# Performance work log

Hardware: AMD Instinct MI355X
Metric: run time of the kernel (lower is better)

The kernel has to match this reference:

```python
import jax, jax.numpy as jnp
import numpy as np

EPS_SINK = 0.01   # SinkhornDistance eps
N_ITERS = 20      # fixed iteration count (original: max 100 with host-side early exit)
BN_EPS = 1e-5


def _conv(x, w, b):
    # NCHW 3x3 (or 1x1) conv, SAME padding
    y = jax.lax.conv_general_dilated(x, w, (1, 1), 'SAME',
                                     dimension_numbers=('NCHW', 'OIHW', 'NCHW'))
    return y + b[None, :, None, None]


def _bn_train(x, gamma, beta):
    # BatchNorm2d in training mode: batch statistics over (N,H,W)
    m = jnp.mean(x, axis=(0, 2, 3), keepdims=True)
    v = jnp.var(x, axis=(0, 2, 3), keepdims=True)
    return gamma[None, :, None, None] * (x - m) * jax.lax.rsqrt(v + BN_EPS) + beta[None, :, None, None]


def _calc_mean_std(f, eps=1e-5):
    m = jnp.mean(f, axis=(2, 3), keepdims=True)
    s = jnp.sqrt(jnp.var(f, axis=(2, 3), keepdims=True) + eps)
    return m, s


def _sinkhorn_pi(x, y, eps):
    # x: [b, n, d] content points, y: [b, m, d] style points. Cosine-distance cost.
    xn = x / jnp.linalg.norm(x, axis=-1, keepdims=True)
    yn = y / jnp.linalg.norm(y, axis=-1, keepdims=True)
    C = 1.0 - jnp.einsum('bnd,bmd->bnm', xn, yn)          # [b, n, m]
    b, n, m = C.shape
    log_mu = jnp.log(jnp.full((b, n), 1.0 / n) + 1e-8)
    log_nu = jnp.log(jnp.full((b, m), 1.0 / m) + 1e-8)

    def Mmat(u, v):
        # (-C + u_i + v_j) / eps
        return (-C + u[..., None] + v[..., None, :]) / eps

    def step(carry, _):
        u, v = carry
        u = eps * (log_mu - jax.scipy.special.logsumexp(Mmat(u, v), axis=-1)) + u
        v = eps * (log_nu - jax.scipy.special.logsumexp(Mmat(u, v), axis=-2)) + v
        return (u, v), None

    (u, v), _ = jax.lax.scan(step, (jnp.zeros((b, n)), jnp.zeros((b, m))), None, length=N_ITERS)
    return jnp.exp(Mmat(u, v))                             # transport plan pi


def setup_inputs() -> dict:
    key = jax.random.key(0)
    ks = jax.random.split(key, 16)
    bs, dim, h, w = 4, 512, 32, 32
    s = 0.05
    return {
        'content_feat': jax.random.normal(ks[0], (bs, dim, h, w), jnp.float32),
        'style_feat':   jax.random.normal(ks[1], (bs, dim, h, w), jnp.float32),
        # alpha_predictor (version 1): conv(1024->256,3x3) ReLU BN, conv(256->256,3x3) ReLU BN, conv(256->512,3x3)
        'w1': jax.random.normal(ks[2], (256, 1024, 3, 3), jnp.float32) * s,
        'b1': jnp.zeros((256,), jnp.float32),
        'g1': jnp.ones((256,), jnp.float32),
        'be1': jnp.zeros((256,), jnp.float32),
        'w2': jax.random.normal(ks[3], (256, 256, 3, 3), jnp.float32) * s,
        'b2': jnp.zeros((256,), jnp.float32),
        'g2': jnp.ones((256,), jnp.float32),
        'be2': jnp.zeros((256,), jnp.float32),
        'w3': jax.random.normal(ks[4], (512, 256, 3, 3), jnp.float32) * s,
        'b3': jnp.zeros((512,), jnp.float32),
        # stand-in decoder head: 3x3 conv 512->3 (decoder is an external injected module)
        'dec_w': jax.random.normal(ks[5], (3, 512, 3, 3), jnp.float32) * s,
        'dec_b': jnp.zeros((3,), jnp.float32),
    }


def reference(content_feat, style_feat, w1, b1, g1, be1, w2, b2, g2, be2, w3, b3, dec_w, dec_b):
    bs, dim, h, w = content_feat.shape
    cf = content_feat.reshape(bs, dim, h * w).transpose(0, 2, 1)   # [b, hw, d]
    sf = style_feat.reshape(bs, dim, h * w).transpose(0, 2, 1)
    pi = _sinkhorn_pi(cf, sf, EPS_SINK) * (h * w)                  # style_assign: pi * h * w
    t = jnp.einsum('bnm,bmd->bnd', pi, sf).transpose(0, 2, 1).reshape(bs, dim, h, w)
    cm, cs = _calc_mean_std(content_feat)
    c_normed = (content_feat - cm) / cs
    a = _bn_train(jax.nn.relu(_conv(jnp.concatenate([t, content_feat], axis=1), w1, b1)), g1, be1)
    a = _bn_train(jax.nn.relu(_conv(a, w2, b2)), g2, be2)
    alpha = _conv(a, w3, b3)
    t = alpha * c_normed + t
    g_t = _conv(t, dec_w, dec_b)
    return g_t
```

## Files before the change

### kernel.cpp

```cpp
#include <hip/hip_runtime.h>

typedef unsigned short u16;
typedef unsigned int u32;
typedef float f32x4 __attribute__((ext_vector_type(4)));
typedef short bf16x8 __attribute__((ext_vector_type(8)));

#define DEV static __device__ __forceinline__

DEV float bf2f(u16 u){ union{float f; u32 i;} x; x.i = ((u32)u) << 16; return x.f; }
DEV u16 f2bf(float f){ union{float f; u32 i;} x; x.f = f; u32 u = x.i;
  return (u16)((u + 0x7fffu + ((u >> 16) & 1u)) >> 16); }
DEV u16 f2h(float f){ _Float16 h = (_Float16)f; u16 u; __builtin_memcpy(&u, &h, 2); return u; }
DEV float h2f(u16 u){ _Float16 h; __builtin_memcpy(&h, &u, 2); return (float)h; }
DEV uint4 pack8(const u16* s){ uint4 v;
  v.x = (u32)s[0] | ((u32)s[1]<<16); v.y = (u32)s[2] | ((u32)s[3]<<16);
  v.z = (u32)s[4] | ((u32)s[5]<<16); v.w = (u32)s[6] | ((u32)s[7]<<16); return v; }
DEV f32x4 mfma16(bf16x8 a, bf16x8 b, f32x4 c){
  return __builtin_amdgcn_mfma_f32_16x16x32_bf16(a, b, c, 0, 0, 0);
}
DEV bf16x8 ldfrag(const u16* p){ return *(const bf16x8*)p; }

constexpr float SCL = 144.269504088896341f;
constexpr float LOG2MU = -9.99998522680257f;

constexpr size_t MB = 1ull << 20;
constexpr size_t OFF_G    = 0;
constexpr size_t OFF_GT   = 8*MB;
constexpr size_t OFF_U    = 16*MB;
constexpr size_t OFF_V    = OFF_U   + (16<<10);
constexpr size_t OFF_INC  = OFF_V   + (16<<10);
constexpr size_t OFF_INS  = OFF_INC + (16<<10);
constexpr size_t OFF_CNM  = OFF_INS + (16<<10);
constexpr size_t OFF_CNIS = OFF_CNM + (8<<10);
constexpr size_t OFF_BNS  = OFF_CNIS+ (8<<10);
constexpr size_t OFF_PNP  = OFF_BNS + (4<<10);
constexpr size_t OFF_CFH  = 17*MB;
constexpr size_t OFF_CFL  = 21*MB;
constexpr size_t OFF_SFH  = 25*MB;
constexpr size_t OFF_SFL  = 29*MB;
constexpr size_t OFF_SNB  = 33*MB;
constexpr size_t OFF_TN   = 37*MB;
constexpr size_t OFF_TCP  = 45*MB;
constexpr size_t OFF_W1P  = 53*MB;
constexpr size_t OFF_W2P  = OFF_W1P + 9*256*1024*2;
constexpr size_t OFF_W3P  = OFF_W2P + 9*256*256*2;
constexpr size_t OFF_WDP  = OFF_W3P + 9*512*256*2;
constexpr size_t OFF_PIP  = 62*MB;
constexpr size_t OFF_Z1  = 17*MB;
constexpr size_t OFF_A1P = 25*MB;
constexpr size_t OFF_Z2  = 27*MB;
constexpr size_t OFF_A2P = 35*MB;
constexpr size_t OFF_T2P = 17*MB;

__global__ void pack_all_k(const float* __restrict__ w1, const float* __restrict__ w2,
                           const float* __restrict__ w3, const float* __restrict__ wd,
                           u16* __restrict__ w1p, u16* __restrict__ w2p,
                           u16* __restrict__ w3p, u16* __restrict__ wdp){
  int blk = blockIdx.x;
  const float* w; u16* wp; int CI, NCK, rel;
  if (blk < 512){ w = w1; wp = w1p; CI = 1024; NCK = 32; rel = blk; }
  else if (blk < 640){ w = w2; wp = w2p; CI = 256; NCK = 8; rel = blk - 512; }
  else if (blk < 896){ w = w3; wp = w3p; CI = 256; NCK = 8; rel = blk - 640; }
  else {
    int o = (blk - 896)*256 + threadIdx.x;
    int ci = o & 511; int r = o >> 9; int co = r & 15; int tap = r >> 4;
    wdp[o] = f2bf((co < 3) ? wd[(size_t)(co*512 + ci)*9 + tap] : 0.f);
    return;
  }
  int g = rel / NCK, ck = rel % NCK;
  __shared__ float L[16*288];
  const float* base = w + ((size_t)(g*16)*CI + ck*32)*9;
  #pragma unroll
  for (int i = 0; i < 18; ++i){
    int idx = i*256 + threadIdx.x;
    int row = idx / 288, col = idx - row*288;
    L[row*288 + col] = base[(size_t)row*CI*9 + col];
  }
  __syncthreads();
  u16* dst = wp + ((size_t)(g*NCK + ck)*9)*512;
  #pragma unroll
  for (int i = 0; i < 18; ++i){
    int j = i*256 + threadIdx.x;
    int tap = j >> 9, r = j & 511, lane = r >> 3, e = r & 7;
    int co = lane & 15, cil = ((lane >> 4) & 3)*8 + e;
    dst[j] = f2bf(L[co*288 + cil*9 + tap]);
  }
}

__global__ void stats_k(const float* __restrict__ cf, const float* __restrict__ sf,
                        float* __restrict__ cnm, float* __restrict__ cnis,
                        float* __restrict__ part, float* __restrict__ zUV,
                        float* __restrict__ zBNS){
  int blk = blockIdx.x;
  if (blk < 2048){
    int bd = blk;
    float4 v = ((const float4*)(cf + (size_t)bd*1024))[threadIdx.x];
    float s = v.x+v.y+v.z+v.w;
    float q = v.x*v.x+v.y*v.y+v.z*v.z+v.w*v.w;
    #pragma unroll
    for (int m = 32; m >= 1; m >>= 1){ s += __shfl_xor(s, m, 64); q += __shfl_xor(q, m, 64); }
    __shared__ float ls[4], lq[4];
    int w = threadIdx.x >> 6;
    if ((threadIdx.x & 63) == 0){ ls[w] = s; lq[w] = q; }
    __syncthreads();
    if (threadIdx.x == 0){
      float S = ls[0]+ls[1]+ls[2]+ls[3], Q = lq[0]+lq[1]+lq[2]+lq[3];
      float mean = S * (1.f/1024.f);
      float var  = Q * (1.f/1024.f) - mean*mean;
      cnm[bd] = mean; cnis[bd] = rsqrtf(var + 1e-5f);
    }
    return;
  }
  if (blk < 2304){
    int rel = blk - 2048;
    int x = rel & 15, y = (rel >> 4) & 7, src = rel >> 7;
    const float* in = src ? sf : cf;
    int p = x*256 + threadIdx.x;
    int b = p >> 10, pp = p & 1023;
    const float* base = in + ((size_t)(b*512 + y*64))*1024 + pp;
    float s = 0.f;
    #pragma unroll 8
    for (int d = 0; d < 64; ++d){ float xx = base[(size_t)d*1024]; s += xx*xx; }
    part[((size_t)(src*8 + y))*4096 + p] = s;
    return;
  }
  if (blk < 2336){
    zUV[(blk - 2304)*256 + threadIdx.x] = 0.f;
    return;
  }
  zBNS[(blk - 2336)*256 + threadIdx.x] = 0.f;
}

__global__ void tsplit_k(const float* __restrict__ cf, const float* __restrict__ sf,
                         const float* __restrict__ pnp,
                         u16* __restrict__ cfh, u16* __restrict__ cfl,
                         u16* __restrict__ sfh, u16* __restrict__ sfl,
                         u16* __restrict__ tcp, u16* __restrict__ snb){
  __shared__ float tile[64][65];
  int z = blockIdx.z, is_style = z >> 2, b = z & 3;
  const float* src = is_style ? sf : cf;
  u16* hi = is_style ? sfh : cfh;
  u16* lo = is_style ? sfl : cfl;
  int p0 = blockIdx.x*64, d0 = blockIdx.y*64;
  int r = threadIdx.x >> 2, c0 = (threadIdx.x & 3) * 16;
  const float* sp = src + ((size_t)(b*512 + d0 + r))*1024 + p0 + c0;
  float v[16];
  #pragma unroll
  for (int e = 0; e < 4; ++e){
    float4 t4 = ((const float4*)sp)[e];
    v[e*4+0]=t4.x; v[e*4+1]=t4.y; v[e*4+2]=t4.z; v[e*4+3]=t4.w;
  }
  #pragma unroll
  for (int j = 0; j < 16; ++j) tile[r][c0+j] = v[j];
  if (is_style){
    u16 t16[16];
    #pragma unroll
    for (int j = 0; j < 16; ++j) t16[j] = f2bf(v[j]);
    uint4* ap = (uint4*)(snb + ((size_t)(b*512 + d0 + r))*1024 + p0 + c0);
    ap[0] = pack8(t16); ap[1] = pack8(t16+8);
  }
  __syncthreads();
  int pr = r, dc0 = c0;
  float inv;
  {
    const float* pp = pnp + (size_t)(is_style ? 8*4096 : 0) + ((b<<10) + p0 + pr);
    float s = 0.f;
    #pragma unroll
    for (int j = 0; j < 8; ++j) s += pp[j*4096];
    inv = rsqrtf(s);
  }
  u16 h16[16], l16[16], t16[16];
  #pragma unroll
  for (int j = 0; j < 16; ++j){
    float x = tile[dc0+j][pr];
    t16[j] = f2bf(x);
    float xn = x * inv;
    u16 h = f2bf(xn);
    h16[j] = h;
    l16[j] = f2bf(xn - bf2f(h));
  }
  size_t orow = (size_t)((b<<10) + p0 + pr);
  uint4* hp = (uint4*)(hi + orow*512 + d0 + dc0);
  uint4* lp = (uint4*)(lo + orow*512 + d0 + dc0);
  hp[0] = pack8(h16); hp[1] = pack8(h16+8);
  lp[0] = pack8(l16); lp[1] = pack8(l16+8);
  if (!is_style){
    int D = d0 + dc0;
    size_t off = ((size_t)(16 + (D>>5))*4096 + orow)*32 + (D&31);
    *(uint4*)(tcp + off)     = pack8(t16);
    *(uint4*)(tcp + off + 8) = pack8(t16+8);
  }
}

__global__ __launch_bounds__(256) void cgemm_k(const u16* __restrict__ cfh, const u16* __restrict__ cfl,
        const u16* __restrict__ sfh, const u16* __restrict__ sfl,
        u16* __restrict__ G, u16* __restrict__ Gt){
  __shared__ __align__(16) u16 SH[4*128*40];
  u16* Ah = SH;          u16* Al = SH + 5120;
  u16* Bh = SH + 10240;  u16* Bl = SH + 15360;
  int b = blockIdx.z;
  size_t abase = ((size_t)((b<<10) + blockIdx.x*128))*512;
  size_t bbase = ((size_t)((b<<10) + blockIdx.y*128))*512;
  int lane = threadIdx.x & 63, wid = threadIdx.x >> 6;
  int wm = (wid >> 1)*64, wn = (wid & 1)*64;
  int fr = lane & 15, qd = lane >> 4;
  int sr = threadIdx.x >> 1, sc = (threadIdx.x & 1)*16;
  f32x4 acc[4][4] = {};
  for (int kk = 0; kk < 512; kk += 32){
    size_t g0 = (size_t)sr*512 + kk + sc;
    *(uint4*)&Ah[sr*40+sc]   = *(const uint4*)(cfh + abase + g0);
    *(uint4*)&Ah[sr*40+sc+8] = *(const uint4*)(cfh + abase + g0 + 8);
    *(uint4*)&Al[sr*40+sc]   = *(const uint4*)(cfl + abase + g0);
    *(uint4*)&Al[sr*40+sc+8] = *(const uint4*)(cfl + abase + g0 + 8);
    *(uint4*)&Bh[sr*40+sc]   = *(const uint4*)(sfh + bbase + g0);
    *(uint4*)&Bh[sr*40+sc+8] = *(const uint4*)(sfh + bbase + g0 + 8);
    *(uint4*)&Bl[sr*40+sc]   = *(const uint4*)(sfl + bbase + g0);
    *(uint4*)&Bl[sr*40+sc+8] = *(const uint4*)(sfl + bbase + g0 + 8);
    __syncthreads();
    bf16x8 bhf[4], blf[4];
    #pragma unroll
    for (int ni = 0; ni < 4; ++ni){
      bhf[ni] = ldfrag(&Bh[(wn + ni*16 + fr)*40 + qd*8]);
      blf[ni] = ldfrag(&Bl[(wn + ni*16 + fr)*40 + qd*8]);
    }
    #pragma unroll
    for (int mi = 0; mi < 4; ++mi){
      bf16x8 ah = ldfrag(&Ah[(wm + mi*16 + fr)*40 + qd*8]);
      bf16x8 al = ldfrag(&Al[(wm + mi*16 + fr)*40 + qd*8]);
      #pragma unroll
      for (int ni = 0; ni < 4; ++ni){
        acc[mi][ni] = mfma16(ah, bhf[ni], acc[mi][ni]);
        acc[mi][ni] = mfma16(ah, blf[ni], acc[mi][ni]);
        acc[mi][ni] = mfma16(al, bhf[ni], acc[mi][ni]);
      }
    }
    __syncthreads();
  }
  #pragma unroll
  for (int mi = 0; mi < 4; ++mi)
    #pragma unroll
    for (int ni = 0; ni < 4; ++ni)
      #pragma unroll
      for (int rg = 0; rg < 4; ++rg){
        int r = wm + mi*16 + qd*4 + rg;
        int c = wn + ni*16 + fr;
        SH[r*136 + c] = f2h((acc[mi][ni][rg] - 1.f) * SCL);
      }
  __syncthreads();
  size_t gb = (((size_t)b) << 20) + (size_t)(blockIdx.x*128)*1024 + blockIdx.y*128;
  #pragma unroll
  for (int i = 0; i < 8; ++i){
    int idx = i*256 + threadIdx.x;
    int r = idx >> 4, c4 = idx & 15;
    *(uint4*)(G + gb + (size_t)r*1024 + c4*8) = *(const uint4*)&SH[r*136 + c4*8];
  }
  __syncthreads();
  #pragma unroll
  for (int mi = 0; mi < 4; ++mi)
    #pragma unroll
    for (int ni = 0; ni < 4; ++ni)
      #pragma unroll
      for (int rg = 0; rg < 4; ++rg){
        int r = wm + mi*16 + qd*4 + rg;
        int c = wn + ni*16 + fr;
        SH[c*136 + r] = f2h((acc[mi][ni][rg] - 1.f) * SCL);
      }
  __syncthreads();
  size_t gtb = (((size_t)b) << 20) + (size_t)(blockIdx.y*128)*1024 + blockIdx.x*128;
  #pragma unroll
  for (int i = 0; i < 8; ++i){
    int idx = i*256 + threadIdx.x;
    int r = idx >> 4, c4 = idx & 15;
    *(uint4*)(Gt + gtb + (size_t)r*1024 + c4*8) = *(const uint4*)&SH[r*136 + c4*8];
  }
}

__global__ void lse_k(const u16* __restrict__ M, const float* __restrict__ addv,
                      float* __restrict__ outv){
  int row = blockIdx.x*4 + (threadIdx.x >> 6);
  int lane = threadIdx.x & 63;
  int b = row >> 10;
  const uint4* r4 = (const uint4*)(M + ((size_t)row << 10));
  const float4* a4 = (const float4*)(addv + ((size_t)b << 10));
  float x[16]; float mx = -3.0e38f;
  #pragma unroll
  for (int e = 0; e < 2; ++e){
    uint4 g = r4[lane + 64*e];
    float4 a0 = a4[2*(lane + 64*e)];
    float4 a1 = a4[2*(lane + 64*e) + 1];
    u32 w[4] = {g.x, g.y, g.z, g.w};
    float av[8] = {a0.x,a0.y,a0.z,a0.w,a1.x,a1.y,a1.z,a1.w};
    #pragma unroll
    for (int i = 0; i < 8; ++i){
      u16 hv = (u16)((i & 1) ? (w[i>>1] >> 16) : (w[i>>1] & 0xffffu));
      float t = h2f(hv) + av[i];
      x[e*8+i] = t;
      mx = fmaxf(mx, t);
    }
  }
  #pragma unroll
  for (int m = 32; m >= 1; m >>= 1) mx = fmaxf(mx, __shfl_xor(mx, m, 64));
  float s = 0.f;
  #pragma unroll
  for (int i = 0; i < 16; ++i) s += exp2f(x[i] - mx);
  #pragma unroll
  for (int m = 32; m >= 1; m >>= 1) s += __shfl_xor(s, m, 64);
  if (lane == 0) outv[row] = LOG2MU - (mx + log2f(s));
}

__global__ void pi_k(const u16* __restrict__ G, const float* __restrict__ U,
                     const float* __restrict__ V, u16* __restrict__ pip){
  int t = threadIdx.x;
  int row = blockIdx.x*2 + (t >> 7);
  int b = row >> 10;
  int j0 = (t & 127) * 8;
  float ur = U[row] + 10.f;
  uint4 g = *(const uint4*)(G + ((size_t)row << 10) + j0);
  const float4* v4 = (const float4*)(V + ((size_t)b << 10) + j0);
  float4 va = v4[0], vb = v4[1];
  u32 gw[4] = {g.x, g.y, g.z, g.w};
  float vv[8] = {va.x,va.y,va.z,va.w,vb.x,vb.y,vb.z,vb.w};
  u16 o[8];
  #pragma unroll
  for (int i = 0; i < 8; ++i){
    u16 hv = (u16)((i & 1) ? (gw[i>>1] >> 16) : (gw[i>>1] & 0xffffu));
    o[i] = f2bf(exp2f(h2f(hv) + vv[i] + ur));
  }
  *(uint4*)(pip + ((size_t)row << 10) + j0) = pack8(o);
}

__global__ __launch_bounds__(256) void tgemm_k(const u16* __restrict__ pip,
        const u16* __restrict__ snb, float* __restrict__ tn, u16* __restrict__ tcp){
  __shared__ __align__(16) u16 As[64*40], Bs[128*40];
  int b = blockIdx.z, p0 = blockIdx.x*64, d0 = blockIdx.y*128;
  int tid = threadIdx.x, lane = tid & 63, wid = tid >> 6;
  int wm = (wid >> 1)*32, wn = (wid & 1)*64;
  int fr = lane & 15, qd = lane >> 4;
  int a_r = tid >> 2, a_c = (tid & 3)*8;
  int b_r = tid >> 1, b_c = (tid & 1)*16;
  const u16* Arow = pip + (((size_t)((b<<10) + p0 + a_r)) << 10) + a_c;
  const u16* Brow = snb + (((size_t)(b*512 + d0 + b_r)) << 10) + b_c;
  uint4 pa, pb0, pb1;
  auto issue = [&](int kk){
    pa = *(const uint4*)(Arow + kk);
    const uint4* bp = (const uint4*)(Brow + kk);
    pb0 = bp[0]; pb1 = bp[1];
  };
  f32x4 acc[2][4] = {};
  issue(0);
  for (int kk = 0; kk < 1024; kk += 32){
    *(uint4*)&As[a_r*40 + a_c] = pa;
    *(uint4*)&Bs[b_r*40 + b_c] = pb0;
    *(uint4*)&Bs[b_r*40 + b_c + 8] = pb1;
    __syncthreads();
    if (kk + 32 < 1024) issue(kk + 32);
    bf16x8 bfr[4];
    #pragma unroll
    for (int ni = 0; ni < 4; ++ni) bfr[ni] = ldfrag(&Bs[(wn + ni*16 + fr)*40 + qd*8]);
    #pragma unroll
    for (int mi = 0; mi < 2; ++mi){
      bf16x8 afr = ldfrag(&As[(wm + mi*16 + fr)*40 + qd*8]);
      #pragma unroll
      for (int ni = 0; ni < 4; ++ni) acc[mi][ni] = mfma16(afr, bfr[ni], acc[mi][ni]);
    }
    __syncthreads();
  }
  #pragma unroll
  for (int mi = 0; mi < 2; ++mi)
    #pragma unroll
    for (int ni = 0; ni < 4; ++ni)
      #pragma unroll
      for (int rg = 0; rg < 4; ++rg){
        int p = p0 + wm + mi*16 + qd*4 + rg;
        int d = d0 + wn + ni*16 + fr;
        float vout = acc[mi][ni][rg];
        size_t ro = (size_t)((b<<10) + p);
        tn[ro*512 + d] = vout;
        tcp[((size_t)(d>>5)*4096 + ro)*32 + (d&31)] = f2bf(vout);
      }
}

template<int CI, int CO, int KSPLIT, int MODE>
__global__ __launch_bounds__(256) void conv_k(const u16* __restrict__ inp, const u16* __restrict__ wpk,
        const float* __restrict__ bias, float* __restrict__ fout, u16* __restrict__ bout,
        const u16* __restrict__ tcp, const float* __restrict__ cnm, const float* __restrict__ cnis,
        const float* __restrict__ tn){
  constexpr int NCK_TOT = CI/32, NCK = NCK_TOT/KSPLIT;
  __shared__ __align__(16) u16 As[128*40];
  int b = blockIdx.z & 3, ks = blockIdx.z >> 2;
  int c0 = blockIdx.y*64;
  int r0 = blockIdx.x*2;
  int tid = threadIdx.x, lane = tid & 63, wid = tid >> 6;
  int wm = (wid >> 1)*32, wn = (wid & 1)*32;
  int fr = lane & 15, qd = lane >> 4;
  int ck0 = ks*NCK;
  int hrow = tid >> 1;
  int ah = (tid & 1)*16;
  int gy = r0 - 1 + (hrow >> 5);
  bool a_ok = ((unsigned)gy < 32u);
  size_t arow = (size_t)(b<<10) + (r0-1)*32 + hrow;
  uint4 pa0 = {0,0,0,0}, pa1 = {0,0,0,0};
  auto issueA = [&](int ck){
    if (a_ok){
      const uint4* s = (const uint4*)(inp + ((size_t)(ck0+ck)*4096 + arow)*32 + ah);
      pa0 = s[0]; pa1 = s[1];
    }
  };
  int g0 = (c0 + wn) >> 4;
  const u16* wb0 = wpk + ((size_t)(g0    )*NCK_TOT + ck0)*9*512 + lane*8;
  const u16* wb1 = wpk + ((size_t)(g0 + 1)*NCK_TOT + ck0)*9*512 + lane*8;

  f32x4 acc[2][2] = {};
  issueA(0);
  for (int ck = 0; ck < NCK; ++ck){
    *(uint4*)&As[hrow*40 + ah]     = pa0;
    *(uint4*)&As[hrow*40 + ah + 8] = pa1;
    __syncthreads();
    if (ck + 1 < NCK) issueA(ck + 1);
    #pragma unroll
    for (int tap = 0; tap < 9; ++tap){
      const int dy = tap/3 - 1, dx = tap%3 - 1;
      bf16x8 bf0 = ldfrag(wb0 + (size_t)(ck*9 + tap)*512);
      bf16x8 bf1 = ldfrag(wb1 + (size_t)(ck*9 + tap)*512);
      #pragma unroll
      for (int mi = 0; mi < 2; ++mi){
        int p0w = wm + mi*16;
        int pcol = (p0w & 31) + fr + dx;
        int lr = (p0w >> 5) + dy + 1;
        bool okc = (unsigned)pcol < 32u;
        bf16x8 af = ldfrag(&As[(lr*32 + (okc ? pcol : 0))*40 + qd*8]);
        if (!okc) af = bf16x8(0);
        acc[mi][0] = mfma16(af, bf0, acc[mi][0]);
        acc[mi][1] = mfma16(af, bf1, acc[mi][1]);
      }
    }
    __syncthreads();
  }
  #pragma unroll
  for (int mi = 0; mi < 2; ++mi)
    #pragma unroll
    for (int ni = 0; ni < 2; ++ni)
      #pragma unroll
      for (int rg = 0; rg < 4; ++rg){
        int pp = blockIdx.x*64 + wm + mi*16 + qd*4 + rg;
        int cc = c0 + wn + ni*16 + fr;
        float v = acc[mi][ni][rg];
        size_t ro = (size_t)((b<<10) + pp);
        if (MODE == 0){
          fout[(size_t)ks*4096*CO + ro*CO + cc] = v;
        } else {
          float alpha = v + bias[cc];
          float cn = (bf2f(tcp[((size_t)(16 + (cc>>5))*4096 + ro)*32 + (cc&31)])
                      - cnm[(b<<9) + cc]) * cnis[(b<<9) + cc];
          bout[((size_t)(cc>>5)*4096 + ro)*32 + (cc&31)] = f2bf(alpha*cn + tn[ro*512 + cc]);
        }
      }
}

__global__ __launch_bounds__(512) void dec_k(const u16* __restrict__ t2p, const u16* __restrict__ wdp,
                                             const float* __restrict__ db, float* __restrict__ out){
  __shared__ float wlds[3*4608];
  int tid = threadIdx.x;
  for (int k = tid; k < 3*4608; k += 512){
    int c = k / 4608, rem = k - c*4608;
    int tap = rem >> 9, ci = rem & 511;
    wlds[k] = bf2f(wdp[(size_t)(tap*16 + c)*512 + ci]);
  }
  __syncthreads();
  int b = blockIdx.x >> 5;
  int p = ((blockIdx.x & 31) << 5) + (tid >> 4);
  int sub = tid & 15;
  int py = p >> 5, px = p & 31;
  float a0 = 0.f, a1 = 0.f, a2 = 0.f;
  for (int tap = 0; tap < 9; ++tap){
    int sy = py + tap/3 - 1, sx = px + tap%3 - 1;
    if (((unsigned)sy < 32u) && ((unsigned)sx < 32u)){
      size_t row = (size_t)((b<<10) + (sy<<5) + sx);
      const float* w0 = wlds + tap*512;
      #pragma unroll
      for (int j = 0; j < 4; ++j){
        int ci0 = j*128 + sub*8;
        uint4 v = *(const uint4*)(t2p + ((size_t)(ci0>>5)*4096 + row)*32 + (ci0&31));
        u32 ww[4] = {v.x, v.y, v.z, v.w};
        #pragma unroll
        for (int e = 0; e < 8; ++e){
          float x = bf2f((u16)((e & 1) ? (ww[e>>1] >> 16) : (ww[e>>1] & 0xffffu)));
          a0 += x * w0[ci0 + e];
          a1 += x * w0[4608 + ci0 + e];
          a2 += x * w0[9216 + ci0 + e];
        }
      }
    }
  }
  #pragma unroll
  for (int m = 8; m >= 1; m >>= 1){
    a0 += __shfl_xor(a0, m, 64);
    a1 += __shfl_xor(a1, m, 64);
    a2 += __shfl_xor(a2, m, 64);
  }
  if (sub == 0){
    out[((size_t)(b*3 + 0) << 10) + p] = a0 + db[0];
    out[((size_t)(b*3 + 1) << 10) + p] = a1 + db[1];
    out[((size_t)(b*3 + 2) << 10) + p] = a2 + db[2];
  }
}

__global__ void bn_stats_k(const float* __restrict__ z, const float* __restrict__ bias,
                           float* __restrict__ sums){
  int c = blockIdx.x*64 + (threadIdx.x & 63);
  int w = threadIdx.x >> 6;
  int rbase = blockIdx.y*512 + w*128;
  float bi = bias[c];
  float s = 0.f, q = 0.f;
  for (int i = 0; i < 128; ++i){
    size_t ro = (size_t)(rbase + i)*256 + c;
    float x = fmaxf(z[ro] + z[4096*256 + ro] + bi, 0.f);
    s += x; q += x*x;
  }
  __shared__ float ls[4][64], lq[4][64];
  ls[w][threadIdx.x & 63] = s; lq[w][threadIdx.x & 63] = q;
  __syncthreads();
  if (threadIdx.x < 64){
    float S = ls[0][threadIdx.x]+ls[1][threadIdx.x]+ls[2][threadIdx.x]+ls[3][threadIdx.x];
    float Q = lq[0][threadIdx.x]+lq[1][threadIdx.x]+lq[2][threadIdx.x]+lq[3][threadIdx.x];
    atomicAdd(&sums[blockIdx.x*64 + threadIdx.x], S);
    atomicAdd(&sums[256 + blockIdx.x*64 + threadIdx.x], Q);
  }
}

__global__ void bn_apply_k(const float* __restrict__ z, const float* __restrict__ bias,
                           const float* __restrict__ sums, const float* __restrict__ gamma,
                           const float* __restrict__ beta, u16* __restrict__ ap){
  int idx = blockIdx.x*256 + threadIdx.x;
  float4 va = ((const float4*)z)[idx];
  float4 vb = ((const float4*)(z + 4096*256))[idx];
  int row = idx >> 6;
  int cc0 = (idx << 2) & 255;
  float e[4] = {va.x+vb.x, va.y+vb.y, va.z+vb.z, va.w+vb.w};
  u16 o[4];
  #pragma unroll
  for (int k = 0; k < 4; ++k){
    int c = cc0 + k;
    float mean = sums[c] * (1.f/4096.f);
    float var  = sums[256 + c] * (1.f/4096.f) - mean*mean;
    float sc = gamma[c] * rsqrtf(var + 1e-5f);
    float sh = beta[c] - mean*sc;
    float x = fmaxf(e[k] + bias[c], 0.f);
    o[k] = f2bf(x*sc + sh);
  }
  uint2 pk; pk.x = (u32)o[0] | ((u32)o[1]<<16); pk.y = (u32)o[2] | ((u32)o[3]<<16);
  *(uint2*)(ap + ((size_t)(cc0>>5)*4096 + row)*32 + (cc0&31)) = pk;
}

extern "C" void kernel_launch(void* const* d_in, const int* in_sizes, int n_in,
                              void* d_out, int out_size, void* d_ws, size_t ws_size,
                              hipStream_t stream){
  const float* cf  = (const float*)d_in[0];
  const float* sf  = (const float*)d_in[1];
  const float* w1  = (const float*)d_in[2];
  const float* b1  = (const float*)d_in[3];
  const float* g1  = (const float*)d_in[4];
  const float* be1 = (const float*)d_in[5];
  const float* w2  = (const float*)d_in[6];
  const float* b2  = (const float*)d_in[7];
  const float* g2  = (const float*)d_in[8];
  const float* be2 = (const float*)d_in[9];
  const float* w3  = (const float*)d_in[10];
  const float* b3  = (const float*)d_in[11];
  const float* dw  = (const float*)d_in[12];
  const float* db  = (const float*)d_in[13];

  char* ws = (char*)d_ws;
  u16* G    = (u16*)(ws + OFF_G);
  u16* Gt   = (u16*)(ws + OFF_GT);
  float* U    = (float*)(ws + OFF_U);
  float* V    = (float*)(ws + OFF_V);
  float* cnm  = (float*)(ws + OFF_CNM);
  float* cnis = (float*)(ws + OFF_CNIS);
  float* bns1 = (float*)(ws + OFF_BNS);
  float* bns2 = bns1 + 512;
  float* pnp  = (float*)(ws + OFF_PNP);
  u16* cfh = (u16*)(ws + OFF_CFH);
  u16* cfl = (u16*)(ws + OFF_CFL);
  u16* sfh = (u16*)(ws + OFF_SFH);
  u16* sfl = (u16*)(ws + OFF_SFL);
  u16* snb = (u16*)(ws + OFF_SNB);
  float* tn  = (float*)(ws + OFF_TN);
  u16* tcp = (u16*)(ws + OFF_TCP);
  u16* w1p = (u16*)(ws + OFF_W1P);
  u16* w2p = (u16*)(ws + OFF_W2P);
  u16* w3p = (u16*)(ws + OFF_W3P);
  u16* wdp = (u16*)(ws + OFF_WDP);
  u16* pip = (u16*)(ws + OFF_PIP);
  float* z1  = (float*)(ws + OFF_Z1);
  u16*   a1p = (u16*)(ws + OFF_A1P);
  float* z2  = (float*)(ws + OFF_Z2);
  u16*   a2p = (u16*)(ws + OFF_A2P);
  u16*   t2p = (u16*)(ws + OFF_T2P);

  pack_all_k<<<1184, 256, 0, stream>>>(w1, w2, w3, dw, w1p, w2p, w3p, wdp);

  stats_k<<<2340, 256, 0, stream>>>(cf, sf, cnm, cnis, pnp, U, bns1);
  tsplit_k<<<dim3(16, 8, 8), 256, 0, stream>>>(cf, sf, pnp, cfh, cfl, sfh, sfl, tcp, snb);

  cgemm_k<<<dim3(8, 8, 4), 256, 0, stream>>>(cfh, cfl, sfh, sfl, G, Gt);

  for (int it = 0; it < 20; ++it){
    lse_k<<<1024, 256, 0, stream>>>(G,  V, U);
    lse_k<<<1024, 256, 0, stream>>>(Gt, U, V);
  }

  pi_k<<<2048, 256, 0, stream>>>(G, U, V, pip);
  tgemm_k<<<dim3(16, 4, 4), 256, 0, stream>>>(pip, snb, tn, tcp);

  conv_k<1024, 256, 2, 0><<<dim3(16, 4, 8), 256, 0, stream>>>(
      tcp, w1p, nullptr, z1, nullptr, nullptr, nullptr, nullptr, nullptr);
  bn_stats_k<<<dim3(4, 8), 256, 0, stream>>>(z1, b1, bns1);
  bn_apply_k<<<1024, 256, 0, stream>>>(z1, b1, bns1, g1, be1, a1p);

  conv_k<256, 256, 2, 0><<<dim3(16, 4, 8), 256, 0, stream>>>(
      a1p, w2p, nullptr, z2, nullptr, nullptr, nullptr, nullptr, nullptr);
  bn_stats_k<<<dim3(4, 8), 256, 0, stream>>>(z2, b2, bns2);
  bn_apply_k<<<1024, 256, 0, stream>>>(z2, b2, bns2, g2, be2, a2p);

  conv_k<256, 512, 1, 1><<<dim3(16, 8, 4), 256, 0, stream>>>(
      a2p, w3p, b3, nullptr, t2p, tcp, cnm, cnis, tn);

  dec_k<<<128, 512, 0, stream>>>(t2p, wdp, db, (float*)d_out);

  (void)in_sizes; (void)n_in; (void)out_size; (void)ws_size;
}
```

Baseline: 406.2 us.

## Fuse Sinkhorn iterations into one persistent kernel with per-batch grid barriers

Replaces the 40 separate log-sum-exp launches and the final pi kernel with a single persistent kernel. Each block keeps its 16-row slices of G and Gt resident in shared memory across all iterations and synchronises with the other blocks of its batch through atomic counter barriers in global memory. This removes the per-launch overhead and the repeated reads of G and Gt from global memory. The risk is that the spin barriers need all 256 blocks to be resident at once, the 64KB of LDS per block limits occupancy, and the barrier latency may dominate.

Result: slower. 541.8 us (+33.4%).

```diff
diff --git a/kernel.cpp b/kernel.cpp
--- a/kernel.cpp
+++ b/kernel.cpp
@@ -28,8 +28,8 @@
 constexpr size_t OFF_GT   = 8*MB;
 constexpr size_t OFF_U    = 16*MB;
 constexpr size_t OFF_V    = OFF_U   + (16<<10);
-constexpr size_t OFF_INC  = OFF_V   + (16<<10);
-constexpr size_t OFF_INS  = OFF_INC + (16<<10);
+constexpr size_t OFF_BAR  = OFF_V   + (16<<10);
+constexpr size_t OFF_INS  = OFF_BAR + (16<<10);
 constexpr size_t OFF_CNM  = OFF_INS + (16<<10);
 constexpr size_t OFF_CNIS = OFF_CNM + (8<<10);
 constexpr size_t OFF_BNS  = OFF_CNIS+ (8<<10);
@@ -90,7 +90,7 @@
 __global__ void stats_k(const float* __restrict__ cf, const float* __restrict__ sf,
                         float* __restrict__ cnm, float* __restrict__ cnis,
                         float* __restrict__ part, float* __restrict__ zUV,
-                        float* __restrict__ zBNS){
+                        float* __restrict__ zBNS, u32* __restrict__ zbar){
   int blk = blockIdx.x;
   if (blk < 2048){
     int bd = blk;
@@ -128,7 +128,11 @@
     zUV[(blk - 2304)*256 + threadIdx.x] = 0.f;
     return;
   }
-  zBNS[(blk - 2336)*256 + threadIdx.x] = 0.f;
+  if (blk < 2340){
+    zBNS[(blk - 2336)*256 + threadIdx.x] = 0.f;
+    return;
+  }
+  zbar[threadIdx.x] = 0u;
 }
 
 __global__ void tsplit_k(const float* __restrict__ cf, const float* __restrict__ sf,
@@ -275,58 +279,102 @@
   }
 }
 
-__global__ void lse_k(const u16* __restrict__ M, const float* __restrict__ addv,
-                      float* __restrict__ outv){
-  int row = blockIdx.x*4 + (threadIdx.x >> 6);
-  int lane = threadIdx.x & 63;
-  int b = row >> 10;
-  const uint4* r4 = (const uint4*)(M + ((size_t)row << 10));
-  const float4* a4 = (const float4*)(addv + ((size_t)b << 10));
-  float x[16]; float mx = -3.0e38f;
-  #pragma unroll
-  for (int e = 0; e < 2; ++e){
-    uint4 g = r4[lane + 64*e];
-    float4 a0 = a4[2*(lane + 64*e)];
-    float4 a1 = a4[2*(lane + 64*e) + 1];
-    u32 w[4] = {g.x, g.y, g.z, g.w};
-    float av[8] = {a0.x,a0.y,a0.z,a0.w,a1.x,a1.y,a1.z,a1.w};
-    #pragma unroll
-    for (int i = 0; i < 8; ++i){
-      u16 hv = (u16)((i & 1) ? (w[i>>1] >> 16) : (w[i>>1] & 0xffffu));
-      float t = h2f(hv) + av[i];
-      x[e*8+i] = t;
-      mx = fmaxf(mx, t);
-    }
-  }
-  #pragma unroll
-  for (int m = 32; m >= 1; m >>= 1) mx = fmaxf(mx, __shfl_xor(mx, m, 64));
-  float s = 0.f;
-  #pragma unroll
-  for (int i = 0; i < 16; ++i) s += exp2f(x[i] - mx);
-  #pragma unroll
-  for (int m = 32; m >= 1; m >>= 1) s += __shfl_xor(s, m, 64);
-  if (lane == 0) outv[row] = LOG2MU - (mx + log2f(s));
-}
-
-__global__ void pi_k(const u16* __restrict__ G, const float* __restrict__ U,
-                     const float* __restrict__ V, u16* __restrict__ pip){
-  int t = threadIdx.x;
-  int row = blockIdx.x*2 + (t >> 7);
-  int b = row >> 10;
-  int j0 = (t & 127) * 8;
-  float ur = U[row] + 10.f;
-  uint4 g = *(const uint4*)(G + ((size_t)row << 10) + j0);
-  const float4* v4 = (const float4*)(V + ((size_t)b << 10) + j0);
-  float4 va = v4[0], vb = v4[1];
-  u32 gw[4] = {g.x, g.y, g.z, g.w};
-  float vv[8] = {va.x,va.y,va.z,va.w,vb.x,vb.y,vb.z,vb.w};
-  u16 o[8];
-  #pragma unroll
-  for (int i = 0; i < 8; ++i){
-    u16 hv = (u16)((i & 1) ? (gw[i>>1] >> 16) : (gw[i>>1] & 0xffffu));
-    o[i] = f2bf(exp2f(h2f(hv) + vv[i] + ur));
-  }
-  *(uint4*)(pip + ((size_t)row << 10) + j0) = pack8(o);
+__global__ __launch_bounds__(512) void sink_k(const u16* __restrict__ G, const u16* __restrict__ Gt,
+        float* __restrict__ U, float* __restrict__ V,
+        u32* __restrict__ bar, u16* __restrict__ pip){
+  __shared__ __align__(16) u16 LL[2][16*1024];
+  int blk = blockIdx.x;
+  int b = blk >> 6;
+  int rb = (blk & 63) << 4;
+  int tid = threadIdx.x;
+  size_t gbase = ((size_t)((b << 10) + rb)) << 10;
+  {
+    const uint4* g0 = (const uint4*)(G + gbase);
+    const uint4* g1 = (const uint4*)(Gt + gbase);
+    uint4* d0 = (uint4*)LL[0];
+    uint4* d1 = (uint4*)LL[1];
+    #pragma unroll
+    for (int i = 0; i < 4; ++i){
+      d0[i*512 + tid] = g0[i*512 + tid];
+      d1[i*512 + tid] = g1[i*512 + tid];
+    }
+  }
+  __syncthreads();
+  int wid = tid >> 6, lane = tid & 63;
+  float* Ub = U + (b << 10);
+  float* Vb = V + (b << 10);
+  u32* barb = bar + b*64;
+  int r0 = wid << 1;
+  int cbase = lane << 2;
+
+  auto dopass = [&](int which, const float* __restrict__ inv, float* __restrict__ outv, int ph){
+    float va[16];
+    #pragma unroll
+    for (int k = 0; k < 4; ++k){
+      float4 t = *(const float4*)(inv + k*256 + cbase);
+      va[k*4+0]=t.x; va[k*4+1]=t.y; va[k*4+2]=t.z; va[k*4+3]=t.w;
+    }
+    #pragma unroll
+    for (int rr = 0; rr < 2; ++rr){
+      int row = r0 + rr;
+      float x[16]; float mx = -3.0e38f;
+      #pragma unroll
+      for (int k = 0; k < 4; ++k){
+        uint2 g2 = *(const uint2*)(&LL[which][row*1024 + k*256 + cbase]);
+        float t0 = h2f((u16)(g2.x & 0xffffu)) + va[k*4+0];
+        float t1 = h2f((u16)(g2.x >> 16))     + va[k*4+1];
+        float t2 = h2f((u16)(g2.y & 0xffffu)) + va[k*4+2];
+        float t3 = h2f((u16)(g2.y >> 16))     + va[k*4+3];
+        x[k*4+0]=t0; x[k*4+1]=t1; x[k*4+2]=t2; x[k*4+3]=t3;
+        mx = fmaxf(mx, fmaxf(fmaxf(t0,t1), fmaxf(t2,t3)));
+      }
+      #pragma unroll
+      for (int m = 32; m >= 1; m >>= 1) mx = fmaxf(mx, __shfl_xor(mx, m, 64));
+      float s = 0.f;
+      #pragma unroll
+      for (int i = 0; i < 16; ++i) s += exp2f(x[i] - mx);
+      #pragma unroll
+      for (int m = 32; m >= 1; m >>= 1) s += __shfl_xor(s, m, 64);
+      if (lane == 0) outv[rb + row] = LOG2MU - (mx + log2f(s));
+    }
+    __syncthreads();
+    if (tid == 0){
+      __hip_atomic_fetch_add(&barb[ph], 1u, __ATOMIC_RELEASE, __HIP_MEMORY_SCOPE_AGENT);
+      while (__hip_atomic_load(&barb[ph], __ATOMIC_RELAXED, __HIP_MEMORY_SCOPE_AGENT) < 64u)
+        __builtin_amdgcn_s_sleep(4);
+      __builtin_amdgcn_fence(__ATOMIC_ACQUIRE, "agent");
+    }
+    __syncthreads();
+  };
+
+  for (int it = 0; it < 20; ++it){
+    dopass(0, Vb, Ub, 2*it);
+    dopass(1, Ub, Vb, 2*it + 1);
+  }
+
+  float va[16];
+  #pragma unroll
+  for (int k = 0; k < 4; ++k){
+    float4 t = *(const float4*)(Vb + k*256 + cbase);
+    va[k*4+0]=t.x; va[k*4+1]=t.y; va[k*4+2]=t.z; va[k*4+3]=t.w;
+  }
+  #pragma unroll
+  for (int rr = 0; rr < 2; ++rr){
+    int row = r0 + rr;
+    float ur = Ub[rb + row] + 10.f;
+    size_t orow = ((size_t)((b << 10) + rb + row)) << 10;
+    #pragma unroll
+    for (int k = 0; k < 4; ++k){
+      uint2 g2 = *(const uint2*)(&LL[0][row*1024 + k*256 + cbase]);
+      u16 o[4];
+      o[0] = f2bf(exp2f(h2f((u16)(g2.x & 0xffffu)) + va[k*4+0] + ur));
+      o[1] = f2bf(exp2f(h2f((u16)(g2.x >> 16))     + va[k*4+1] + ur));
+      o[2] = f2bf(exp2f(h2f((u16)(g2.y & 0xffffu)) + va[k*4+2] + ur));
+      o[3] = f2bf(exp2f(h2f((u16)(g2.y >> 16))     + va[k*4+3] + ur));
+      uint2 pk; pk.x = (u32)o[0] | ((u32)o[1]<<16); pk.y = (u32)o[2] | ((u32)o[3]<<16);
+      *(uint2*)(pip + orow + k*256 + cbase) = pk;
+    }
+  }
 }
 
 __global__ __launch_bounds__(256) void tgemm_k(const u16* __restrict__ pip,
@@ -575,6 +623,7 @@
   u16* Gt   = (u16*)(ws + OFF_GT);
   float* U    = (float*)(ws + OFF_U);
   float* V    = (float*)(ws + OFF_V);
+  u32* bar    = (u32*)(ws + OFF_BAR);
   float* cnm  = (float*)(ws + OFF_CNM);
   float* cnis = (float*)(ws + OFF_CNIS);
   float* bns1 = (float*)(ws + OFF_BNS);
@@ -600,17 +649,13 @@
 
   pack_all_k<<<1184, 256, 0, stream>>>(w1, w2, w3, dw, w1p, w2p, w3p, wdp);
 
-  stats_k<<<2340, 256, 0, stream>>>(cf, sf, cnm, cnis, pnp, U, bns1);
+  stats_k<<<2341, 256, 0, stream>>>(cf, sf, cnm, cnis, pnp, U, bns1, bar);
   tsplit_k<<<dim3(16, 8, 8), 256, 0, stream>>>(cf, sf, pnp, cfh, cfl, sfh, sfl, tcp, snb);
 
   cgemm_k<<<dim3(8, 8, 4), 256, 0, stream>>>(cfh, cfl, sfh, sfl, G, Gt);
 
-  for (int it = 0; it < 20; ++it){
-    lse_k<<<1024, 256, 0, stream>>>(G,  V, U);
-    lse_k<<<1024, 256, 0, stream>>>(Gt, U, V);
-  }
-
-  pi_k<<<2048, 256, 0, stream>>>(G, U, V, pip);
+  sink_k<<<256, 512, 0, stream>>>(G, Gt, U, V, bar, pip);
+
   tgemm_k<<<dim3(16, 4, 4), 256, 0, stream>>>(pip, snb, tn, tcp);
 
   conv_k<1024, 256, 2, 0><<<dim3(16, 4, 8), 256, 0, stream>>>(
```
